# Kernel tuning notes

Hardware: AMD Instinct MI355X
Metric: run time of the kernel (lower is better)

Reference implementation:

```python
import jax, jax.numpy as jnp
import numpy as np
import math

B, L, IN_K, IN_V = 4, 2048, 256, 256
HID, HEADS, OUT = 1024, 8, 256
D = HID // HEADS  # head_dim = 128


def setup_inputs() -> dict:
    key = jax.random.key(0)
    ks = jax.random.split(key, 9)
    s = 0.02
    return {
        "KEY": jax.random.normal(ks[0], (B, L, IN_K), jnp.float32),
        "VALUE": jax.random.normal(ks[1], (B, L, IN_V), jnp.float32),
        "QUERY": jax.random.normal(ks[2], (B, L, IN_K), jnp.float32),
        "W_w": jax.random.normal(ks[3], (HID, IN_K), jnp.float32) * s,
        "W_b": jax.random.normal(ks[4], (HID,), jnp.float32) * s,
        "Wv_w": jax.random.normal(ks[5], (HID, IN_V), jnp.float32) * s,
        "Wv_b": jax.random.normal(ks[6], (HID,), jnp.float32) * s,
        "Wo_w": jax.random.normal(ks[7], (OUT, HID), jnp.float32) * s,
        "Wo_b": jax.random.normal(ks[8], (OUT,), jnp.float32) * s,
    }


def _split_heads(x, b, l):
    # reshape hidden -> (head_dim, num_heads) [head LAST, as in source], then
    # permute(0,3,1,2) -> [B, heads, L, head_dim]
    return x.reshape(b, l, D, HEADS).transpose(0, 3, 1, 2)


def reference(KEY, VALUE, QUERY, W_w, W_b, Wv_w, Wv_b, Wo_w, Wo_b):
    b, lk, _ = KEY.shape
    lq = QUERY.shape[1]
    # shared projection W for KEY and QUERY
    Wk = _split_heads(KEY @ W_w.T + W_b, b, lk)      # [B,h,Lk,d]
    Wq = _split_heads(QUERY @ W_w.T + W_b, b, lq)    # [B,h,Lq,d]
    Wv = _split_heads(VALUE @ Wv_w.T + Wv_b, b, lk)  # [B,h,Lk,d]
    # score[b,h,i,k] = sum_j Wk[b,h,i,j] * Wq[b,h,k,j]
    score = jnp.einsum('bhij,bhkj->bhik', Wk, Wq) / math.sqrt(D)
    # NON-STANDARD: softmax over the HEAD dimension (dim=1)
    attn = jax.nn.softmax(score, axis=1)             # [B,h,Lk,Lq]
    out = jnp.einsum('bhik,bhij->bhjk', attn, Wv)    # [B,h,d,Lq]
    out = out.transpose(0, 2, 1, 3)                  # [B,d,h,Lq]
    out = out.reshape(b, D * HEADS, lq)              # [B,hidden,Lq]
    out = jnp.swapaxes(out, 2, 1)                    # [B,Lq,hidden]
    # dropout is identity in eval mode
    return out @ Wo_w.T + Wo_b                       # [B,Lq,output_size]
```

## Files before the change

### kernel.cpp

```cpp
#include <hip/hip_runtime.h>
#include <hip/hip_bf16.h>
#include <stdint.h>

#define B_    4
#define L_    2048
#define INK   256
#define HID   1024
#define NH    8
#define DH    128
#define OUTF  256

typedef __bf16 v8bf __attribute__((ext_vector_type(8)));
typedef float  v4f  __attribute__((ext_vector_type(4)));

#define MFMA(a,b,c) __builtin_amdgcn_mfma_f32_16x16x32_bf16((a),(b),(c),0,0,0)

__device__ __forceinline__ void gl_lds16(const void* gsrc, void* ldsbase) {
  __builtin_amdgcn_global_load_lds(
      (const __attribute__((address_space(1))) unsigned int*)(uintptr_t)gsrc,
      (__attribute__((address_space(3))) unsigned int*)(uint32_t)(uintptr_t)ldsbase,
      16, 0, 0);
}
__device__ __forceinline__ void sched_fence() { asm volatile("" ::: "memory"); }
__device__ __forceinline__ void barrier_lgkm() {
  asm volatile("s_waitcnt lgkmcnt(0)\n\ts_barrier" ::: "memory");
}

__device__ __forceinline__ unsigned short bfbits(float f) {
  __bf16 h = (__bf16)f;
  return __builtin_bit_cast(unsigned short, h);
}
__device__ __forceinline__ unsigned pack2(float a, float b) {
  return (unsigned)bfbits(a) | ((unsigned)bfbits(b) << 16);
}

struct ConvArgs {
  const float* src[5];
  __bf16* dst[5];
  int n[5];
};
__global__ __launch_bounds__(256)
void convert_kernel(ConvArgs a) {
  const int r = blockIdx.y;
  const int i = (blockIdx.x * 256 + threadIdx.x) * 4;
  if (i >= a.n[r]) return;
  const float4 v = *(const float4*)(a.src[r] + i);
  uint2 w;
  w.x = pack2(v.x, v.y);
  w.y = pack2(v.z, v.w);
  *reinterpret_cast<uint2*>(a.dst[r] + i) = w;
}

__global__ __launch_bounds__(256)
void wo_perm_kernel(const float* __restrict__ Wo, __bf16* __restrict__ Wop) {
  const int o = blockIdx.x;
  const int hidp = threadIdx.x * 4;
  const int h = hidp >> 7, dd = hidp & 127;
  const float* src = Wo + (size_t)o * HID;
  const float v0 = src[(dd + 0) * 8 + h];
  const float v1 = src[(dd + 1) * 8 + h];
  const float v2 = src[(dd + 2) * 8 + h];
  const float v3 = src[(dd + 3) * 8 + h];
  uint2 w;
  w.x = pack2(v0, v1);
  w.y = pack2(v2, v3);
  *reinterpret_cast<uint2*>(Wop + (size_t)o * HID + hidp) = w;
}

template<int MODE>
__global__ __launch_bounds__(256, 2)
void proj_kernel(const __bf16* __restrict__ X, const __bf16* __restrict__ W,
                 const float* __restrict__ bias, float scale,
                 __bf16* __restrict__ out)
{
  __shared__ __bf16 sA[2][128 * 64];
  __shared__ __bf16 sB[2][128 * 64];
  const int tid  = threadIdx.x;
  const int lane = tid & 63;
  const int wid  = tid >> 6;
  const int l15  = lane & 15;
  const int q    = lane >> 4;
  const int mblk = blockIdx.x * 128;
  const int nblk = blockIdx.y * 128;

  v4f acc[4][4];
  const v4f vz = {0.f, 0.f, 0.f, 0.f};
#pragma unroll
  for (int i = 0; i < 4; i++)
#pragma unroll
    for (int j = 0; j < 4; j++) acc[i][j] = vz;

  const char* Ab = (const char*)X + (size_t)mblk * 512;
  const char* Bb = (const char*)W + (size_t)nblk * 512;

  auto stage = [&](int p, int c) {
    const int koff = c * 128;
#pragma unroll
    for (int j = 0; j < 4; j++) {
      const int slot = j * 256 + tid;
      const int row = slot >> 3, g = slot & 7;
      gl_lds16(Ab + (size_t)row * 512 + koff + ((g ^ (row & 7)) << 4),
               &sA[p][(j * 256 + wid * 64) * 8]);
    }
#pragma unroll
    for (int j = 0; j < 4; j++) {
      const int slot = j * 256 + tid;
      const int row = slot >> 3, g = slot & 7;
      gl_lds16(Bb + (size_t)row * 512 + koff + ((g ^ (row & 7)) << 4),
               &sB[p][(j * 256 + wid * 64) * 8]);
    }
  };

  stage(0, 0);
  __syncthreads();
#pragma unroll
  for (int c = 0; c < 4; c++) {
    const int p = c & 1;
    if (c + 1 < 4) stage(1 - p, c + 1);
#pragma unroll
    for (int s = 0; s < 2; s++) {
      v8bf a[4], b[4];
#pragma unroll
      for (int t = 0; t < 4; t++) {
        const int row = (wid & 1) * 64 + t * 16 + l15;
        a[t] = *(const v8bf*)&sA[p][(row << 6) + (((s * 4 + q) ^ (row & 7)) << 3)];
      }
#pragma unroll
      for (int t = 0; t < 4; t++) {
        const int row = (wid >> 1) * 64 + t * 16 + l15;
        b[t] = *(const v8bf*)&sB[p][(row << 6) + (((s * 4 + q) ^ (row & 7)) << 3)];
      }
#pragma unroll
      for (int tm = 0; tm < 4; tm++)
#pragma unroll
        for (int tn = 0; tn < 4; tn++)
          acc[tm][tn] = MFMA(a[tm], b[tn], acc[tm][tn]);
    }
    __syncthreads();
  }

#pragma unroll
  for (int tn = 0; tn < 4; tn++) {
    const int n = nblk + (wid >> 1) * 64 + tn * 16 + l15;
    const float bv = bias[n];
    const int h = n & 7;
    const int dd = n >> 3;
#pragma unroll
    for (int tm = 0; tm < 4; tm++)
#pragma unroll
      for (int r = 0; r < 4; r++) {
        const int m = mblk + (wid & 1) * 64 + tm * 16 + q * 4 + r;
        const int b = m >> 11;
        const int i = m & (L_ - 1);
        const float v = (acc[tm][tn][r] + bv) * scale;
        size_t idx;
        if (MODE == 0) {
          idx = ((size_t)(b * NH + h) * L_ + i) * DH + dd;
        } else {
          const int ii = (i >> 3) & 3;
          idx = ((size_t)(b * NH + h) * 64 + (i >> 5)) * 4096 +
                (ii * 128 + dd) * 8 + (i & 7);
        }
        out[idx] = (__bf16)v;
      }
  }
}

__global__ __launch_bounds__(512, 2)
void fused_attn_kernel(const __bf16* __restrict__ Kp,
                       const __bf16* __restrict__ Qp,
                       const __bf16* __restrict__ Vg,
                       __bf16* __restrict__ Hd)
{
  extern __shared__ char smem[];
  char* sPf = smem;
  char* sPn = smem + 40960;

  const int tid  = threadIdx.x;
  const int lane = tid & 63;
  const int h    = tid >> 6;
  const int l15  = lane & 15;
  const int q    = lane >> 4;
  const int k0   = blockIdx.x * 32;
  const int b    = blockIdx.y;

  const char* KpH = (const char*)Kp + (size_t)(b * NH + h) * L_ * DH * 2;
  const char* QpH = (const char*)Qp + (size_t)(b * NH + h) * L_ * DH * 2;
  const char* VgH = (const char*)Vg + (size_t)(b * NH + h) * 64 * 8192;
  char* sPfH = sPf + h * 5120;
  char* sPnH = sPn + h * 2560;

  auto loadKa = [&](v8bf (&ka)[2][4], int it) {
    const char* base = KpH + (size_t)it * 32 * 256;
#pragma unroll
    for (int si = 0; si < 2; si++)
#pragma unroll
      for (int c = 0; c < 4; c++)
        ka[si][c] = *(const v8bf*)(base + (si * 16 + l15) * 256 + (c * 4 + q) * 16);
  };
  auto loadVa = [&](v8bf (&va)[8], int it) {
    const char* base = VgH + (size_t)it * 8192 + q * 2048;
#pragma unroll
    for (int t = 0; t < 8; t++)
      va[t] = *(const v8bf*)(base + (t * 16 + l15) * 16);
  };

  v8bf qf[2][4];
#pragma unroll
  for (int n = 0; n < 2; n++)
#pragma unroll
    for (int c = 0; c < 4; c++)
      qf[n][c] = *(const v8bf*)(QpH + (size_t)(k0 + n * 16 + l15) * 256 + c * 64 + q * 16);

  v8bf ka[2][4];
  loadKa(ka, 0);

  v4f cacc[8][2];
  const v4f vz = {0.f, 0.f, 0.f, 0.f};
#pragma unroll
  for (int t = 0; t < 8; t++)
#pragma unroll
    for (int n = 0; n < 2; n++) cacc[t][n] = vz;

  const int ip = tid & 15;
  const int kk = tid >> 4;

#pragma unroll 1
  for (int it = 0; it < 64; ++it) {
    v8bf va[8];
    loadVa(va, it);
    sched_fence();

    v4f s[2][2];
#pragma unroll
    for (int si = 0; si < 2; si++)
#pragma unroll
      for (int n = 0; n < 2; n++) s[si][n] = vz;
#pragma unroll
    for (int c = 0; c < 4; c++)
#pragma unroll
      for (int si = 0; si < 2; si++)
#pragma unroll
        for (int n = 0; n < 2; n++)
          s[si][n] = MFMA(ka[si][c], qf[n][c], s[si][n]);

    if (it + 1 < 64) loadKa(ka, it + 1);

#pragma unroll
    for (int si = 0; si < 2; si++)
#pragma unroll
      for (int n = 0; n < 2; n++) {
        v4f p;
#pragma unroll
        for (int r = 0; r < 4; r++) p[r] = exp2f(s[si][n][r]);
        *(v4f*)(sPfH + (n * 16 + l15) * 160 + si * 64 + q * 16) = p;
      }
    barrier_lgkm();

    {
      float2 vals[8];
      float s0 = 0.f, s1 = 0.f;
#pragma unroll
      for (int hh = 0; hh < 8; hh++) {
        vals[hh] = *(const float2*)(sPf + hh * 5120 + kk * 160 + ip * 8);
        s0 += vals[hh].x;
        s1 += vals[hh].y;
      }
      const float r0 = __builtin_amdgcn_rcpf(s0);
      const float r1 = __builtin_amdgcn_rcpf(s1);
#pragma unroll
      for (int hh = 0; hh < 8; hh++)
        *(unsigned*)(sPn + hh * 2560 + kk * 80 + ip * 4) =
            pack2(vals[hh].x * r0, vals[hh].y * r1);
    }
    barrier_lgkm();

    v8bf pb[2];
#pragma unroll
    for (int n = 0; n < 2; n++)
      pb[n] = *(const v8bf*)(sPnH + (n * 16 + l15) * 80 + q * 16);
#pragma unroll
    for (int t = 0; t < 8; t++)
#pragma unroll
      for (int n = 0; n < 2; n++)
        cacc[t][n] = MFMA(va[t], pb[n], cacc[t][n]);
  }

#pragma unroll
  for (int t = 0; t < 8; t++)
#pragma unroll
    for (int n = 0; n < 2; n++) {
      uint2 w;
      w.x = pack2(cacc[t][n][0], cacc[t][n][1]);
      w.y = pack2(cacc[t][n][2], cacc[t][n][3]);
      char* dst = (char*)Hd +
          (((size_t)(b * L_ + k0 + n * 16 + l15)) * HID + h * DH + t * 16 + q * 4) * 2;
      *(uint2*)dst = w;
    }
}

__global__ __launch_bounds__(256, 2)
void outproj_kernel(const __bf16* __restrict__ Hd, const __bf16* __restrict__ Wop,
                    const float* __restrict__ bo, float* __restrict__ out)
{
  __shared__ __bf16 sA[2][64 * 64];
  __shared__ __bf16 sB[2][64 * 64];
  const int tid  = threadIdx.x;
  const int lane = tid & 63;
  const int wid  = tid >> 6;
  const int l15  = lane & 15;
  const int q    = lane >> 4;
  const int mblk = blockIdx.x * 64;
  const int nblk = blockIdx.y * 64;

  const char* Ab = (const char*)Hd  + (size_t)mblk * 2048;
  const char* Bb = (const char*)Wop + (size_t)nblk * 2048;

  auto stage = [&](int p, int c) {
#pragma unroll
    for (int j = 0; j < 2; j++) {
      const int slot = j * 256 + tid;
      const int row = slot >> 3, g = slot & 7;
      gl_lds16(Ab + (size_t)row * 2048 + c * 128 + ((g ^ (row & 7)) << 4),
               &sA[p][(j * 256 + wid * 64) * 8]);
    }
#pragma unroll
    for (int j = 0; j < 2; j++) {
      const int slot = j * 256 + tid;
      const int row = slot >> 3, g = slot & 7;
      gl_lds16(Bb + (size_t)row * 2048 + c * 128 + ((g ^ (row & 7)) << 4),
               &sB[p][(j * 256 + wid * 64) * 8]);
    }
  };

  v4f acc[2][2];
  const v4f vz = {0.f, 0.f, 0.f, 0.f};
#pragma unroll
  for (int i = 0; i < 2; i++)
#pragma unroll
    for (int j = 0; j < 2; j++) acc[i][j] = vz;

  stage(0, 0);
  __syncthreads();
#pragma unroll 1
  for (int c = 0; c < 16; c++) {
    const int p = c & 1;
    if (c + 1 < 16) stage(1 - p, c + 1);
#pragma unroll
    for (int s = 0; s < 2; s++) {
      v8bf a[2], bb[2];
#pragma unroll
      for (int t = 0; t < 2; t++) {
        const int row = (wid & 1) * 32 + t * 16 + l15;
        a[t] = *(const v8bf*)&sA[p][(row << 6) + (((s * 4 + q) ^ (row & 7)) << 3)];
      }
#pragma unroll
      for (int t = 0; t < 2; t++) {
        const int row = (wid >> 1) * 32 + t * 16 + l15;
        bb[t] = *(const v8bf*)&sB[p][(row << 6) + (((s * 4 + q) ^ (row & 7)) << 3)];
      }
#pragma unroll
      for (int tm = 0; tm < 2; tm++)
#pragma unroll
        for (int tn = 0; tn < 2; tn++)
          acc[tm][tn] = MFMA(a[tm], bb[tn], acc[tm][tn]);
    }
    __syncthreads();
  }

#pragma unroll
  for (int tn = 0; tn < 2; tn++) {
    const int n = nblk + (wid >> 1) * 32 + tn * 16 + l15;
    const float bv = bo[n];
#pragma unroll
    for (int tm = 0; tm < 2; tm++)
#pragma unroll
      for (int r = 0; r < 4; r++) {
        const int m = mblk + (wid & 1) * 32 + tm * 16 + q * 4 + r;
        out[(size_t)m * OUTF + n] = acc[tm][tn][r] + bv;
      }
  }
}

extern "C" void kernel_launch(void* const* d_in, const int* in_sizes, int n_in,
                              void* d_out, int out_size, void* d_ws, size_t ws_size,
                              hipStream_t stream) {
  const float* KEY   = (const float*)d_in[0];
  const float* VALUE = (const float*)d_in[1];
  const float* QUERY = (const float*)d_in[2];
  const float* W_w   = (const float*)d_in[3];
  const float* W_b   = (const float*)d_in[4];
  const float* Wv_w  = (const float*)d_in[5];
  const float* Wv_b  = (const float*)d_in[6];
  const float* Wo_w  = (const float*)d_in[7];
  const float* Wo_b  = (const float*)d_in[8];
  float* out = (float*)d_out;

  const size_t MB = 1024 * 1024;
  char* ws = (char*)d_ws;
  __bf16* Kp  = (__bf16*)(ws);
  __bf16* Qp  = (__bf16*)(ws + 16 * MB);
  __bf16* Vg  = (__bf16*)(ws + 32 * MB);
  __bf16* Hd  = (__bf16*)(ws + 48 * MB);
  __bf16* Wop = (__bf16*)(ws + 64 * MB);
  __bf16* Xk  = (__bf16*)(ws + 48 * MB);
  __bf16* Xq  = (__bf16*)(ws + 48 * MB + 4 * MB);
  __bf16* Xv  = (__bf16*)(ws + 48 * MB + 8 * MB);
  __bf16* Wb  = (__bf16*)(ws + 48 * MB + 12 * MB);
  __bf16* Wvb = (__bf16*)(ws + 48 * MB + 12 * MB + 512 * 1024);

  ConvArgs ca;
  ca.src[0] = KEY;   ca.dst[0] = Xk;  ca.n[0] = B_ * L_ * INK;
  ca.src[1] = QUERY; ca.dst[1] = Xq;  ca.n[1] = B_ * L_ * INK;
  ca.src[2] = VALUE; ca.dst[2] = Xv;  ca.n[2] = B_ * L_ * INK;
  ca.src[3] = W_w;   ca.dst[3] = Wb;  ca.n[3] = HID * INK;
  ca.src[4] = Wv_w;  ca.dst[4] = Wvb; ca.n[4] = HID * INK;
  convert_kernel<<<dim3(2048, 5), 256, 0, stream>>>(ca);
  wo_perm_kernel<<<dim3(256), 256, 0, stream>>>(Wo_w, Wop);

  const float c2 = 0.12751744f;
  proj_kernel<0><<<dim3(64, 8), 256, 0, stream>>>(Xk, Wb,  W_b,  1.0f, Kp);
  proj_kernel<0><<<dim3(64, 8), 256, 0, stream>>>(Xq, Wb,  W_b,  c2,   Qp);
  proj_kernel<1><<<dim3(64, 8), 256, 0, stream>>>(Xv, Wvb, Wv_b, 1.0f, Vg);

  fused_attn_kernel<<<dim3(64, B_), 512, 61440, stream>>>(Kp, Qp, Vg, Hd);

  outproj_kernel<<<dim3(128, 4), 256, 0, stream>>>(Hd, Wop, Wo_b, out);
}
```

Before: 326.6 us.

## Split attention over key halves, merge partials in out-projection, batch projections

The attention kernel now processes 64 query columns per block and splits the key loop into two halves across a new grid dimension. Each half writes its own partial output buffer, and the out-projection kernel loads both and sums them in bf16. The three projection launches are merged into one z-indexed launch. Softmax probabilities are now stored once as bf16 in a swizzled LDS layout that is normalised in place, which shrinks LDS use and drops the separate fp32 buffer. In exchange the kernel keeps more accumulators live, loses the K/V prefetch overlap, and adds precision loss from bf16 exponentials and from summing the partials in bf16.

```diff
diff --git a/kernel.cpp b/kernel.cpp
--- a/kernel.cpp
+++ b/kernel.cpp
@@ -21,7 +21,6 @@
       (__attribute__((address_space(3))) unsigned int*)(uint32_t)(uintptr_t)ldsbase,
       16, 0, 0);
 }
-__device__ __forceinline__ void sched_fence() { asm volatile("" ::: "memory"); }
 __device__ __forceinline__ void barrier_lgkm() {
   asm volatile("s_waitcnt lgkmcnt(0)\n\ts_barrier" ::: "memory");
 }
@@ -32,6 +31,12 @@
 }
 __device__ __forceinline__ unsigned pack2(float a, float b) {
   return (unsigned)bfbits(a) | ((unsigned)bfbits(b) << 16);
+}
+__device__ __forceinline__ float bflo(unsigned u) {
+  return __builtin_bit_cast(float, u << 16);
+}
+__device__ __forceinline__ float bfhi(unsigned u) {
+  return __builtin_bit_cast(float, u & 0xFFFF0000u);
 }
 
 struct ConvArgs {
@@ -67,14 +72,26 @@
   *reinterpret_cast<uint2*>(Wop + (size_t)o * HID + hidp) = w;
 }
 
-template<int MODE>
+struct ProjArgs {
+  const __bf16* X[3];
+  const __bf16* W[3];
+  const float*  bias[3];
+  float scale[3];
+  __bf16* out[3];
+};
 __global__ __launch_bounds__(256, 2)
-void proj_kernel(const __bf16* __restrict__ X, const __bf16* __restrict__ W,
-                 const float* __restrict__ bias, float scale,
-                 __bf16* __restrict__ out)
+void proj_kernel(ProjArgs pa)
 {
   __shared__ __bf16 sA[2][128 * 64];
   __shared__ __bf16 sB[2][128 * 64];
+  const int z = blockIdx.z;
+  const __bf16* X = pa.X[z];
+  const __bf16* W = pa.W[z];
+  const float* bias = pa.bias[z];
+  const float scale = pa.scale[z];
+  __bf16* out = pa.out[z];
+  const int mode = (z == 2);
+
   const int tid  = threadIdx.x;
   const int lane = tid & 63;
   const int wid  = tid >> 6;
@@ -154,7 +171,7 @@
         const int i = m & (L_ - 1);
         const float v = (acc[tm][tn][r] + bv) * scale;
         size_t idx;
-        if (MODE == 0) {
+        if (mode == 0) {
           idx = ((size_t)(b * NH + h) * L_ + i) * DH + dd;
         } else {
           const int ii = (i >> 3) & 3;
@@ -170,126 +187,139 @@
 void fused_attn_kernel(const __bf16* __restrict__ Kp,
                        const __bf16* __restrict__ Qp,
                        const __bf16* __restrict__ Vg,
-                       __bf16* __restrict__ Hd)
+                       __bf16* __restrict__ Hd0,
+                       __bf16* __restrict__ Hd1)
 {
-  extern __shared__ char smem[];
-  char* sPf = smem;
-  char* sPn = smem + 40960;
+  __shared__ char sPe[32768];
 
   const int tid  = threadIdx.x;
   const int lane = tid & 63;
   const int h    = tid >> 6;
   const int l15  = lane & 15;
   const int q    = lane >> 4;
-  const int k0   = blockIdx.x * 32;
-  const int b    = blockIdx.y;
+  const int k0   = blockIdx.x * 64;
+  const int ih   = blockIdx.y;
+  const int b    = blockIdx.z;
 
   const char* KpH = (const char*)Kp + (size_t)(b * NH + h) * L_ * DH * 2;
   const char* QpH = (const char*)Qp + (size_t)(b * NH + h) * L_ * DH * 2;
   const char* VgH = (const char*)Vg + (size_t)(b * NH + h) * 64 * 8192;
-  char* sPfH = sPf + h * 5120;
-  char* sPnH = sPn + h * 2560;
-
-  auto loadKa = [&](v8bf (&ka)[2][4], int it) {
-    const char* base = KpH + (size_t)it * 32 * 256;
-#pragma unroll
-    for (int si = 0; si < 2; si++)
+  char* sPh = sPe + h * 4096;
+  __bf16* Hd = ih ? Hd1 : Hd0;
+
+  v8bf qf[2][2][4];
+#pragma unroll
+  for (int ks = 0; ks < 2; ks++)
+#pragma unroll
+    for (int n = 0; n < 2; n++)
 #pragma unroll
       for (int c = 0; c < 4; c++)
-        ka[si][c] = *(const v8bf*)(base + (si * 16 + l15) * 256 + (c * 4 + q) * 16);
-  };
-  auto loadVa = [&](v8bf (&va)[8], int it) {
-    const char* base = VgH + (size_t)it * 8192 + q * 2048;
-#pragma unroll
-    for (int t = 0; t < 8; t++)
-      va[t] = *(const v8bf*)(base + (t * 16 + l15) * 16);
-  };
-
-  v8bf qf[2][4];
-#pragma unroll
-  for (int n = 0; n < 2; n++)
-#pragma unroll
-    for (int c = 0; c < 4; c++)
-      qf[n][c] = *(const v8bf*)(QpH + (size_t)(k0 + n * 16 + l15) * 256 + c * 64 + q * 16);
-
-  v8bf ka[2][4];
-  loadKa(ka, 0);
-
-  v4f cacc[8][2];
+        qf[ks][n][c] = *(const v8bf*)(QpH +
+            (size_t)(k0 + ks * 32 + n * 16 + l15) * 256 + c * 64 + q * 16);
+
+  v4f cacc[8][4];
   const v4f vz = {0.f, 0.f, 0.f, 0.f};
 #pragma unroll
   for (int t = 0; t < 8; t++)
 #pragma unroll
-    for (int n = 0; n < 2; n++) cacc[t][n] = vz;
-
-  const int ip = tid & 15;
-  const int kk = tid >> 4;
-
+    for (int n = 0; n < 4; n++) cacc[t][n] = vz;
+
+  const int it0 = ih * 32;
 #pragma unroll 1
-  for (int it = 0; it < 64; ++it) {
+  for (int itl = 0; itl < 32; ++itl) {
+    const int it = it0 + itl;
+
+    v8bf ka[2][4];
+    {
+      const char* base = KpH + (size_t)it * 32 * 256;
+#pragma unroll
+      for (int si = 0; si < 2; si++)
+#pragma unroll
+        for (int c = 0; c < 4; c++)
+          ka[si][c] = *(const v8bf*)(base + (si * 16 + l15) * 256 + (c * 4 + q) * 16);
+    }
+
+#pragma unroll
+    for (int ks = 0; ks < 2; ks++) {
+      v4f s[2][2];
+#pragma unroll
+      for (int si = 0; si < 2; si++)
+#pragma unroll
+        for (int n = 0; n < 2; n++) s[si][n] = vz;
+#pragma unroll
+      for (int c = 0; c < 4; c++)
+#pragma unroll
+        for (int si = 0; si < 2; si++)
+#pragma unroll
+          for (int n = 0; n < 2; n++)
+            s[si][n] = MFMA(ka[si][c], qf[ks][n][c], s[si][n]);
+#pragma unroll
+      for (int si = 0; si < 2; si++)
+#pragma unroll
+        for (int n = 0; n < 2; n++) {
+          const int kb = ks * 32 + n * 16 + l15;
+          const int gi = si * 4 + q;
+          uint2 w;
+          w.x = pack2(exp2f(s[si][n][0]), exp2f(s[si][n][1]));
+          w.y = pack2(exp2f(s[si][n][2]), exp2f(s[si][n][3]));
+          *(uint2*)(sPh + kb * 64 + ((gi ^ (kb & 6)) << 3)) = w;
+        }
+    }
+    barrier_lgkm();
+
     v8bf va[8];
-    loadVa(va, it);
-    sched_fence();
-
-    v4f s[2][2];
-#pragma unroll
-    for (int si = 0; si < 2; si++)
-#pragma unroll
-      for (int n = 0; n < 2; n++) s[si][n] = vz;
-#pragma unroll
-    for (int c = 0; c < 4; c++)
-#pragma unroll
-      for (int si = 0; si < 2; si++)
-#pragma unroll
-        for (int n = 0; n < 2; n++)
-          s[si][n] = MFMA(ka[si][c], qf[n][c], s[si][n]);
-
-    if (it + 1 < 64) loadKa(ka, it + 1);
-
-#pragma unroll
-    for (int si = 0; si < 2; si++)
-#pragma unroll
-      for (int n = 0; n < 2; n++) {
-        v4f p;
-#pragma unroll
-        for (int r = 0; r < 4; r++) p[r] = exp2f(s[si][n][r]);
-        *(v4f*)(sPfH + (n * 16 + l15) * 160 + si * 64 + q * 16) = p;
-      }
-    barrier_lgkm();
-
     {
-      float2 vals[8];
-      float s0 = 0.f, s1 = 0.f;
+      const char* base = VgH + (size_t)it * 8192 + q * 2048;
+#pragma unroll
+      for (int t = 0; t < 8; t++)
+        va[t] = *(const v8bf*)(base + (t * 16 + l15) * 16);
+    }
+
+    {
+      const int kk = tid >> 3;
+      const int i4 = tid & 7;
+      const int off = kk * 64 + ((i4 ^ (kk & 6)) << 3);
+      uint2 u[8];
+      float s0 = 0.f, s1 = 0.f, s2 = 0.f, s3 = 0.f;
 #pragma unroll
       for (int hh = 0; hh < 8; hh++) {
-        vals[hh] = *(const float2*)(sPf + hh * 5120 + kk * 160 + ip * 8);
-        s0 += vals[hh].x;
-        s1 += vals[hh].y;
+        u[hh] = *(const uint2*)(sPe + hh * 4096 + off);
+        s0 += bflo(u[hh].x);
+        s1 += bfhi(u[hh].x);
+        s2 += bflo(u[hh].y);
+        s3 += bfhi(u[hh].y);
       }
       const float r0 = __builtin_amdgcn_rcpf(s0);
       const float r1 = __builtin_amdgcn_rcpf(s1);
-#pragma unroll
-      for (int hh = 0; hh < 8; hh++)
-        *(unsigned*)(sPn + hh * 2560 + kk * 80 + ip * 4) =
-            pack2(vals[hh].x * r0, vals[hh].y * r1);
+      const float r2 = __builtin_amdgcn_rcpf(s2);
+      const float r3 = __builtin_amdgcn_rcpf(s3);
+#pragma unroll
+      for (int hh = 0; hh < 8; hh++) {
+        uint2 w;
+        w.x = pack2(bflo(u[hh].x) * r0, bfhi(u[hh].x) * r1);
+        w.y = pack2(bflo(u[hh].y) * r2, bfhi(u[hh].y) * r3);
+        *(uint2*)(sPe + hh * 4096 + off) = w;
+      }
     }
     barrier_lgkm();
 
-    v8bf pb[2];
-#pragma unroll
-    for (int n = 0; n < 2; n++)
-      pb[n] = *(const v8bf*)(sPnH + (n * 16 + l15) * 80 + q * 16);
+    v8bf pb[4];
+#pragma unroll
+    for (int n = 0; n < 4; n++) {
+      const int kb = n * 16 + l15;
+      pb[n] = *(const v8bf*)(sPh + kb * 64 + (((q * 2) ^ (kb & 6)) << 3));
+    }
 #pragma unroll
     for (int t = 0; t < 8; t++)
 #pragma unroll
-      for (int n = 0; n < 2; n++)
+      for (int n = 0; n < 4; n++)
         cacc[t][n] = MFMA(va[t], pb[n], cacc[t][n]);
   }
 
 #pragma unroll
   for (int t = 0; t < 8; t++)
 #pragma unroll
-    for (int n = 0; n < 2; n++) {
+    for (int n = 0; n < 4; n++) {
       uint2 w;
       w.x = pack2(cacc[t][n][0], cacc[t][n][1]);
       w.y = pack2(cacc[t][n][2], cacc[t][n][3]);
@@ -299,12 +329,21 @@
     }
 }
 
+__device__ __forceinline__ v8bf add8(v8bf a, v8bf b) {
+  v8bf r;
+#pragma unroll
+  for (int i = 0; i < 8; i++) r[i] = (__bf16)((float)a[i] + (float)b[i]);
+  return r;
+}
+
 __global__ __launch_bounds__(256, 2)
-void outproj_kernel(const __bf16* __restrict__ Hd, const __bf16* __restrict__ Wop,
+void outproj_kernel(const __bf16* __restrict__ Hd0, const __bf16* __restrict__ Hd1,
+                    const __bf16* __restrict__ Wop,
                     const float* __restrict__ bo, float* __restrict__ out)
 {
-  __shared__ __bf16 sA[2][64 * 64];
-  __shared__ __bf16 sB[2][64 * 64];
+  __shared__ __bf16 sA0[2][64 * 64];
+  __shared__ __bf16 sA1[2][64 * 64];
+  __shared__ __bf16 sB [2][64 * 64];
   const int tid  = threadIdx.x;
   const int lane = tid & 63;
   const int wid  = tid >> 6;
@@ -313,23 +352,19 @@
   const int mblk = blockIdx.x * 64;
   const int nblk = blockIdx.y * 64;
 
-  const char* Ab = (const char*)Hd  + (size_t)mblk * 2048;
-  const char* Bb = (const char*)Wop + (size_t)nblk * 2048;
+  const char* A0b = (const char*)Hd0 + (size_t)mblk * 2048;
+  const char* A1b = (const char*)Hd1 + (size_t)mblk * 2048;
+  const char* Bb  = (const char*)Wop + (size_t)nblk * 2048;
 
   auto stage = [&](int p, int c) {
 #pragma unroll
     for (int j = 0; j < 2; j++) {
       const int slot = j * 256 + tid;
       const int row = slot >> 3, g = slot & 7;
-      gl_lds16(Ab + (size_t)row * 2048 + c * 128 + ((g ^ (row & 7)) << 4),
-               &sA[p][(j * 256 + wid * 64) * 8]);
-    }
-#pragma unroll
-    for (int j = 0; j < 2; j++) {
-      const int slot = j * 256 + tid;
-      const int row = slot >> 3, g = slot & 7;
-      gl_lds16(Bb + (size_t)row * 2048 + c * 128 + ((g ^ (row & 7)) << 4),
-               &sB[p][(j * 256 + wid * 64) * 8]);
+      const size_t goff = (size_t)row * 2048 + c * 128 + ((g ^ (row & 7)) << 4);
+      gl_lds16(A0b + goff, &sA0[p][(j * 256 + wid * 64) * 8]);
+      gl_lds16(A1b + goff, &sA1[p][(j * 256 + wid * 64) * 8]);
+      gl_lds16(Bb  + goff, &sB [p][(j * 256 + wid * 64) * 8]);
     }
   };
 
@@ -352,7 +387,8 @@
 #pragma unroll
       for (int t = 0; t < 2; t++) {
         const int row = (wid & 1) * 32 + t * 16 + l15;
-        a[t] = *(const v8bf*)&sA[p][(row << 6) + (((s * 4 + q) ^ (row & 7)) << 3)];
+        const int off = (row << 6) + (((s * 4 + q) ^ (row & 7)) << 3);
+        a[t] = add8(*(const v8bf*)&sA0[p][off], *(const v8bf*)&sA1[p][off]);
       }
 #pragma unroll
       for (int t = 0; t < 2; t++) {
@@ -401,8 +437,9 @@
   __bf16* Kp  = (__bf16*)(ws);
   __bf16* Qp  = (__bf16*)(ws + 16 * MB);
   __bf16* Vg  = (__bf16*)(ws + 32 * MB);
-  __bf16* Hd  = (__bf16*)(ws + 48 * MB);
-  __bf16* Wop = (__bf16*)(ws + 64 * MB);
+  __bf16* Hd0 = (__bf16*)(ws + 48 * MB);
+  __bf16* Hd1 = (__bf16*)(ws + 64 * MB);
+  __bf16* Wop = (__bf16*)(ws + 80 * MB);
   __bf16* Xk  = (__bf16*)(ws + 48 * MB);
   __bf16* Xq  = (__bf16*)(ws + 48 * MB + 4 * MB);
   __bf16* Xv  = (__bf16*)(ws + 48 * MB + 8 * MB);
@@ -419,11 +456,13 @@
   wo_perm_kernel<<<dim3(256), 256, 0, stream>>>(Wo_w, Wop);
 
   const float c2 = 0.12751744f;
-  proj_kernel<0><<<dim3(64, 8), 256, 0, stream>>>(Xk, Wb,  W_b,  1.0f, Kp);
-  proj_kernel<0><<<dim3(64, 8), 256, 0, stream>>>(Xq, Wb,  W_b,  c2,   Qp);
-  proj_kernel<1><<<dim3(64, 8), 256, 0, stream>>>(Xv, Wvb, Wv_b, 1.0f, Vg);
-
-  fused_attn_kernel<<<dim3(64, B_), 512, 61440, stream>>>(Kp, Qp, Vg, Hd);
-
-  outproj_kernel<<<dim3(128, 4), 256, 0, stream>>>(Hd, Wop, Wo_b, out);
-}
+  ProjArgs pa;
+  pa.X[0] = Xk;  pa.W[0] = Wb;  pa.bias[0] = W_b;  pa.scale[0] = 1.0f; pa.out[0] = Kp;
+  pa.X[1] = Xq;  pa.W[1] = Wb;  pa.bias[1] = W_b;  pa.scale[1] = c2;   pa.out[1] = Qp;
+  pa.X[2] = Xv;  pa.W[2] = Wvb; pa.bias[2] = Wv_b; pa.scale[2] = 1.0f; pa.out[2] = Vg;
+  proj_kernel<<<dim3(64, 8, 3), 256, 0, stream>>>(pa);
+
+  fused_attn_kernel<<<dim3(32, 2, B_), 512, 0, stream>>>(Kp, Qp, Vg, Hd0, Hd1);
+
+  outproj_kernel<<<dim3(128, 4), 256, 0, stream>>>(Hd0, Hd1, Wop, Wo_b, out);
+}
```

Result: faster. 312.4 us (-4.4%).
